# Optimization experiments

Hardware: AMD Instinct MI355X
Metric: run time of the kernel (lower is better)

The kernel has to match this reference:

```python
import jax, jax.numpy as jnp
import numpy as np

SCALES = (32.0, 64.0, 128.0, 256.0)
RATIOS = (0.5, 1.0, 2.0)
STRIDE = 16
KEEP = 2000          # pre-NMS top-k
TOPK = 300           # post-NMS top-k
MIN_SIZE = 16.0
SCORE_THRESH = 0.05
NMS_THRESH = 0.7


def static_anchors():
    a = []
    for s in SCALES:
        for r in RATIOS:
            w = s * r ** 0.5
            h = s / r ** 0.5
            a.append((-w / 2, -h / 2, w / 2, h / 2))
    return jnp.asarray(a, jnp.float32)  # [12,4]


def generate_anchors(h, w):
    base = static_anchors()
    sx = jnp.arange(w, dtype=jnp.float32) * STRIDE + STRIDE / 2
    sy = jnp.arange(h, dtype=jnp.float32) * STRIDE + STRIDE / 2
    yy, xx = jnp.meshgrid(sy, sx, indexing='ij')
    xs, ys = xx.reshape(-1), yy.reshape(-1)
    shifts = jnp.stack((xs, ys, xs, ys), axis=1)            # [HW,4]
    return (base[None, :, :] + shifts[:, None, :]).reshape(-1, 4)  # [HW*12,4]


def apply_deltas(anchors, d):
    # bbox reg weights are all 1.0
    aw = anchors[..., 2] - anchors[..., 0]
    ah = anchors[..., 3] - anchors[..., 1]
    ax = anchors[..., 0] + aw * 0.5
    ay = anchors[..., 1] + ah * 0.5
    x = ax + d[..., 0] * aw
    y = ay + d[..., 1] * ah
    w = aw * jnp.exp(d[..., 2])
    h = ah * jnp.exp(d[..., 3])
    return jnp.stack((x - w * 0.5, y - h * 0.5, x + w * 0.5, y + h * 0.5), axis=-1)


def conv2d(x, w, b, pad):
    y = jax.lax.conv_general_dilated(x, w, (1, 1), [(pad, pad), (pad, pad)],
                                     dimension_numbers=('NCHW', 'OIHW', 'NCHW'))
    return y + b[None, :, None, None]


def nms_fixed(boxes, scores, valid):
    # boxes already sorted by descending score; greedy NMS with fixed shapes.
    area = (boxes[:, 2] - boxes[:, 0]) * (boxes[:, 3] - boxes[:, 1])
    lt = jnp.maximum(boxes[:, None, :2], boxes[None, :, :2])
    rb = jnp.minimum(boxes[:, None, 2:], boxes[None, :, 2:])
    wh = jnp.clip(rb - lt, 0.0)
    inter = wh[..., 0] * wh[..., 1]
    iou = inter / jnp.maximum(area[:, None] + area[None, :] - inter, 1e-6)
    n = boxes.shape[0]

    def body(i, state):
        keep, supp = state
        k = jnp.logical_and(~supp[i], True)
        keep = keep.at[i].set(k)
        supp = jnp.logical_or(supp, jnp.logical_and(k, iou[i] > NMS_THRESH))
        return keep, supp

    keep, _ = jax.lax.fori_loop(0, n, body, (jnp.zeros(n, bool), ~valid))
    masked = jnp.where(keep, scores, -jnp.inf)
    top_s, top_i = jax.lax.top_k(masked, TOPK)
    ok = top_s > -jnp.inf
    out_boxes = jnp.where(ok[:, None], boxes[top_i], 0.0)
    out_scores = jnp.where(ok, top_s, 0.0)
    return out_boxes, out_scores


def rpn_forward(fx, w1, b1, w2, b2, w3, b3, img_h, img_w):
    _, _, H, W = fx.shape
    x = jax.nn.relu(conv2d(fx, w1, b1, 1))        # [1,512,H,W]
    ox = conv2d(x, w2, b2, 0)                     # [1,12,H,W]
    ax = conv2d(x, w3, b3, 0)                     # [1,48,H,W]
    anchors = generate_anchors(H, W)              # [A,4]
    ox = jnp.transpose(ox, (0, 2, 3, 1)).reshape(-1)                     # [A]
    ax = jnp.transpose(ax.reshape(1, 12, 4, H, W), (0, 3, 4, 1, 2)).reshape(-1, 4)  # [A,4]
    px = apply_deltas(anchors, ax)                # [A,4]
    s = jax.nn.sigmoid(ox)
    top_s, idx = jax.lax.top_k(s, KEEP)           # pre-NMS filter
    b = px[idx]
    x1 = jnp.clip(b[:, 0], 0.0, img_w)
    x2 = jnp.clip(b[:, 2], 0.0, img_w)
    y1 = jnp.clip(b[:, 1], 0.0, img_h)
    y2 = jnp.clip(b[:, 3], 0.0, img_h)
    boxes = jnp.stack((x1, y1, x2, y2), axis=1)
    valid = ((x2 - x1) >= MIN_SIZE) & ((y2 - y1) >= MIN_SIZE) & (top_s >= SCORE_THRESH)
    out_boxes, out_scores = nms_fixed(boxes, top_s, valid)
    return jnp.concatenate((out_boxes, out_scores[:, None]), axis=1)  # [TOPK,5]


def setup_inputs() -> dict:
    key = jax.random.key(0)
    ks = jax.random.split(key, 4)
    fx = jax.random.normal(ks[0], (1, 1024, 64, 64), jnp.float32)
    w1 = jax.random.normal(ks[1], (512, 1024, 3, 3), jnp.float32) * 0.01
    w2 = jax.random.normal(ks[2], (12, 512, 1, 1), jnp.float32) * 0.01
    w3 = jax.random.normal(ks[3], (48, 512, 1, 1), jnp.float32) * 0.01
    return {"fx": fx, "w1": w1, "b1": jnp.zeros((512,), jnp.float32),
            "w2": w2, "b2": jnp.zeros((12,), jnp.float32),
            "w3": w3, "b3": jnp.zeros((48,), jnp.float32),
            "img_h": 1024, "img_w": 1024}


def reference(fx, w1, b1, w2, b2, w3, b3, img_h, img_w):
    return rpn_forward(fx, w1, b1, w2, b2, w3, b3, float(img_h), float(img_w))
```

## Files before the change

kernel.cpp:

```cpp
#include <hip/hip_runtime.h>
#include <math.h>

typedef unsigned int u32;
typedef unsigned long long u64;
typedef unsigned short u16;

typedef float f32x16 __attribute__((ext_vector_type(16)));
typedef short bf16x8 __attribute__((ext_vector_type(8)));

#define A_TOTAL 49152
#define NKEEP 2000
#define NTOPK 300
#define SORTN 4096

#define OFF_PACC   0u
#define OFF_SCORES 16777216u
#define OFF_HIST   16973824u
#define OFF_KEYS   17235968u
#define OFF_CAND5  17268736u
#define OFF_MASK   17309696u
#define OFF_BOX4   17833984u
#define OFF_MISC   17899520u
#define OFF_PREW   17903616u
#define OFF_POX    17903616u
#define WS_NEED    46215168ull

__global__ __launch_bounds__(256) void k_init(u32* __restrict__ hist, u64* __restrict__ keys,
                                              u32* __restrict__ misc, float* __restrict__ out) {
    int t = blockIdx.x * 256 + threadIdx.x;
    if (t < 65536) hist[t] = 0u;
    if (t < SORTN) keys[t] = 0ull;
    if (t < NTOPK * 5) out[t] = 0.f;
    if (t == 0) misc[0] = 0u;
}

__device__ __forceinline__ u16 f2bf(float v) {
    u32 u = __float_as_uint(v);
    return (u16)((u + 0x7FFFu + ((u >> 16) & 1u)) >> 16);
}
__device__ __forceinline__ float bf2f(u16 h) { return __uint_as_float(((u32)h) << 16); }
__device__ __forceinline__ void split3(float v, u16& h, u16& m, u16& l) {
    h = f2bf(v);
    float r1 = v - bf2f(h);
    m = f2bf(r1);
    float r2 = r1 - bf2f(m);
    l = f2bf(r2);
}
__device__ __forceinline__ bf16x8 ldsfrag(const u16* p) {
    const u64* q = (const u64*)p;
    union { u64 w[2]; bf16x8 v; } x;
    x.w[0] = q[0];
    x.w[1] = q[1];
    return x.v;
}
__device__ __forceinline__ void gll16(const void* g, void* l) {
    __builtin_amdgcn_global_load_lds((const __attribute__((address_space(1))) void*)g,
                                     (__attribute__((address_space(3))) void*)l, 16, 0, 0);
}
__device__ __forceinline__ void gll4(const void* g, void* l) {
    __builtin_amdgcn_global_load_lds((const __attribute__((address_space(1))) void*)g,
                                     (__attribute__((address_space(3))) void*)l, 4, 0, 0);
}

__global__ __launch_bounds__(256) void k_splitw(const float* __restrict__ w1, uint4* __restrict__ preW) {
    __shared__ __align__(16) u16 sW[3 * 9216];
    const int tid = threadIdx.x;
    const int c = blockIdx.x;
    const int yb = blockIdx.y;
    const int kh = blockIdx.z;
    const float* base = w1 + (size_t)(yb * 64) * 9216 + (size_t)(kh * 512 + c * 16) * 9;
#pragma unroll
    for (int j = 0; j < 36; j++) {
        int e = tid + j * 256;
        int co = e / 144, r = e - co * 144;
        int ci = r / 9, tap = r - ci * 9;
        float v = base[(size_t)co * 9216 + r];
        u16 h, m, l;
        split3(v, h, m, l);
        int li = ((tap * 2 + (ci >> 3)) * 64 + co) * 8 + (ci & 7);
        sW[li] = h; sW[9216 + li] = m; sW[18432 + li] = l;
    }
    __syncthreads();
    const uint4* sw4 = (const uint4*)sW;
    uint4* dst = preW + (size_t)(((kh * 8 + yb) * 32 + c) * 3) * 1152;
#pragma unroll
    for (int j = 0; j < 14; j++) {
        int e = tid + j * 256;
        if (e < 3456) dst[e] = sw4[e];
    }
}

__global__ __launch_bounds__(512) void k_conv1m(const float* __restrict__ fx, const uint4* __restrict__ preW,
                                                float* __restrict__ pacc) {
    __shared__ __align__(16) u16 sA[3 * 9216];
    __shared__ __align__(16) u16 sB[3 * 3600];
    u32* const sB32 = (u32*)sB;
    const int tid = threadIdx.x;
    const int lane = tid & 63;
    const int wid = tid >> 6;
    const int cgw = wid >> 2;
    const int pgw = wid & 3;
    const int n = lane & 31;
    const int g = lane >> 5;
    const int bid = blockIdx.x;
    const int yb = bid & 7;
    const int rest = bid >> 3;
    const int bpx = rest & 31;
    const int kh = rest >> 5;
    const int y0 = (bpx >> 2) * 8, x0 = (bpx & 3) * 16;
    const int ci_base = kh * 512;

    int fgp[3], flp[3];
    bool wrp[3], ldp[3];
#pragma unroll
    for (int j = 0; j < 3; j++) {
        int p = tid + j * 512;
        bool wr = p < 1440;
        int a = p / 180, rem = p - a * 180;
        int hy = rem / 18, hx = rem - hy * 18;
        int gy = y0 + hy - 1, gx = x0 + hx - 1;
        bool ok = wr && gy >= 0 && gy < 64 && gx >= 0 && gx < 64;
        wrp[j] = wr;
        ldp[j] = ok;
        fgp[j] = ok ? ((2 * a) * 4096 + gy * 64 + gx) : 0;
        flp[j] = wr ? (rem * 10 + a) : 0;
    }

    f32x16 acc;
    double accD[16];
#pragma unroll
    for (int i = 0; i < 16; i++) { acc[i] = 0.f; accD[i] = 0.0; }

    float pA0[3], pA1[3], pB0[3], pB1[3];
    {
        const float* f0 = fx + (size_t)ci_base * 4096;
        const float* f1 = fx + (size_t)(ci_base + 16) * 4096;
#pragma unroll
        for (int j = 0; j < 3; j++) {
            pA0[j] = ldp[j] ? f0[fgp[j]] : 0.f;
            pA1[j] = ldp[j] ? f0[fgp[j] + 4096] : 0.f;
            pB0[j] = ldp[j] ? f1[fgp[j]] : 0.f;
            pB1[j] = ldp[j] ? f1[fgp[j] + 4096] : 0.f;
        }
    }
    const char* wbase = (const char*)preW + (size_t)((kh * 8 + yb) * 32) * 3 * 18432;
    char* const sAc = (char*)sA;

#pragma unroll 1
    for (int c = 0; c < 32; c++) {
        __syncthreads();
        const char* wsrc = wbase + (size_t)c * 3 * 18432;
#pragma unroll
        for (int s = 0; s < 3; s++) {
            gll16(wsrc + s * 18432 + tid * 16,         sAc + s * 18432 + wid * 1024);
            gll16(wsrc + s * 18432 + 8192 + tid * 16,  sAc + s * 18432 + 8192 + wid * 1024);
            gll4 (wsrc + s * 18432 + 16384 + tid * 4,  sAc + s * 18432 + 16384 + wid * 256);
        }
#pragma unroll
        for (int j = 0; j < 3; j++) {
            if (wrp[j]) {
                u16 h0, m0, l0, h1, m1, l1;
                split3(pA0[j], h0, m0, l0);
                split3(pA1[j], h1, m1, l1);
                sB32[flp[j]] = (u32)h0 | ((u32)h1 << 16);
                sB32[1800 + flp[j]] = (u32)m0 | ((u32)m1 << 16);
                sB32[3600 + flp[j]] = (u32)l0 | ((u32)l1 << 16);
            }
        }
        __syncthreads();
#pragma unroll
        for (int j = 0; j < 3; j++) { pA0[j] = pB0[j]; pA1[j] = pB1[j]; }
        if (c < 30) {
            const float* fp = fx + (size_t)(ci_base + (c + 2) * 16) * 4096;
#pragma unroll
            for (int j = 0; j < 3; j++) {
                pB0[j] = ldp[j] ? fp[fgp[j]] : 0.f;
                pB1[j] = ldp[j] ? fp[fgp[j] + 4096] : 0.f;
            }
        }

#pragma unroll 1
        for (int dy = 0; dy < 3; dy++) {
#pragma unroll
            for (int dx = 0; dx < 3; dx++) {
                const int tap = dy * 3 + dx;
                const int aoff = ((tap * 2 + g) * 64 + cgw * 32 + n) * 8;
                bf16x8 ah = ldsfrag(&sA[aoff]);
                bf16x8 am = ldsfrag(&sA[9216 + aoff]);
                bf16x8 al = ldsfrag(&sA[18432 + aoff]);
                const int loc = (pgw * 2 + (n >> 4) + dy) * 18 + (n & 15) + dx;
                const int boff = loc * 20 + g * 8;
                bf16x8 bh = ldsfrag(&sB[boff]);
                bf16x8 bm = ldsfrag(&sB[3600 + boff]);
                bf16x8 bl = ldsfrag(&sB[7200 + boff]);
                acc = __builtin_amdgcn_mfma_f32_32x32x16_bf16(ah, bh, acc, 0, 0, 0);
                acc = __builtin_amdgcn_mfma_f32_32x32x16_bf16(ah, bm, acc, 0, 0, 0);
                acc = __builtin_amdgcn_mfma_f32_32x32x16_bf16(am, bh, acc, 0, 0, 0);
                acc = __builtin_amdgcn_mfma_f32_32x32x16_bf16(ah, bl, acc, 0, 0, 0);
                acc = __builtin_amdgcn_mfma_f32_32x32x16_bf16(am, bm, acc, 0, 0, 0);
                acc = __builtin_amdgcn_mfma_f32_32x32x16_bf16(al, bh, acc, 0, 0, 0);
            }
#pragma unroll
            for (int i = 0; i < 16; i++) { accD[i] += (double)acc[i]; acc[i] = 0.f; }
        }
    }

    {
        int p = pgw * 32 + n;
        int py = p >> 4, pxx = p & 15;
        int gp = (y0 + py) * 64 + x0 + pxx;
        const int row_hi = 4 * g;
#pragma unroll
        for (int rg = 0; rg < 16; rg++) {
            int co = yb * 64 + cgw * 32 + (rg & 3) + 8 * (rg >> 2) + row_hi;
            pacc[(size_t)kh * 2097152 + (size_t)co * 4096 + gp] = (float)accD[rg];
        }
    }
}

__global__ __launch_bounds__(512) void k_conv1m_fb(const float* __restrict__ fx, const float* __restrict__ w1,
                                                   float* __restrict__ pacc) {
    __shared__ u16 sA[3 * 9472];
    __shared__ u16 sB[3 * 3600];
    u32* const sA32 = (u32*)sA;
    const int tid = threadIdx.x;
    const int lane = tid & 63;
    const int wid = tid >> 6;
    const int cgw = wid >> 2;
    const int pgw = wid & 3;
    const int n = lane & 31;
    const int g = lane >> 5;
    const int bid = blockIdx.x;
    const int yb = bid & 7;
    const int rest = bid >> 3;
    const int bpx = rest & 31;
    const int kh = rest >> 5;
    const int y0 = (bpx >> 2) * 8, x0 = (bpx & 3) * 16;
    const int co0 = yb * 64;
    const int ci_base = kh * 512;

    int wgp[9], wlp[9];
#pragma unroll
    for (int j = 0; j < 9; j++) {
        int p = tid + j * 512;
        int co = p / 72, q = p - co * 72;
        int a = q & 7, b = q >> 3;
        wgp[j] = co * 9216 + (2 * a) * 9 + b;
        wlp[j] = co * 74 + b * 8 + a;
    }
    int fg0[6], fl[6];
#pragma unroll
    for (int j = 0; j < 6; j++) {
        int idx = tid + j * 512;
        bool wr = idx < 2880;
        int ci = idx / 180, rem = idx - ci * 180;
        int hy = rem / 18, hx = rem - hy * 18;
        int gy = y0 + hy - 1, gx = x0 + hx - 1;
        bool ok = wr && gy >= 0 && gy < 64 && gx >= 0 && gx < 64;
        fg0[j] = ok ? (ci * 4096 + gy * 64 + gx) : -1;
        fl[j] = wr ? (rem * 20 + ci) : -1;
    }

    f32x16 acc;
    double accD[16];
#pragma unroll
    for (int i = 0; i < 16; i++) { acc[i] = 0.f; accD[i] = 0.0; }

    float pw[18], pfA[6], pfB[6];
    {
        const float* wp = w1 + (size_t)co0 * 9216 + (size_t)ci_base * 9;
#pragma unroll
        for (int j = 0; j < 9; j++) { pw[2 * j] = wp[wgp[j]]; pw[2 * j + 1] = wp[wgp[j] + 9]; }
        const float* f0 = fx + (size_t)ci_base * 4096;
        const float* f1 = fx + (size_t)(ci_base + 16) * 4096;
#pragma unroll
        for (int j = 0; j < 6; j++) {
            pfA[j] = (fg0[j] >= 0) ? f0[fg0[j]] : 0.f;
            pfB[j] = (fg0[j] >= 0) ? f1[fg0[j]] : 0.f;
        }
    }

#pragma unroll 1
    for (int c = 0; c < 32; c++) {
        __syncthreads();
#pragma unroll
        for (int j = 0; j < 9; j++) {
            u16 h0, m0, l0, h1, m1, l1;
            split3(pw[2 * j], h0, m0, l0);
            split3(pw[2 * j + 1], h1, m1, l1);
            sA32[wlp[j]] = (u32)h0 | ((u32)h1 << 16);
            sA32[4736 + wlp[j]] = (u32)m0 | ((u32)m1 << 16);
            sA32[9472 + wlp[j]] = (u32)l0 | ((u32)l1 << 16);
        }
#pragma unroll
        for (int j = 0; j < 6; j++) {
            if (fl[j] >= 0) {
                u16 h, m, l;
                split3(pfA[j], h, m, l);
                sB[fl[j]] = h; sB[3600 + fl[j]] = m; sB[7200 + fl[j]] = l;
            }
        }
        __syncthreads();
        if (c < 31) {
            const float* wp = w1 + (size_t)co0 * 9216 + (size_t)(ci_base + (c + 1) * 16) * 9;
#pragma unroll
            for (int j = 0; j < 9; j++) { pw[2 * j] = wp[wgp[j]]; pw[2 * j + 1] = wp[wgp[j] + 9]; }
        }
#pragma unroll
        for (int j = 0; j < 6; j++) pfA[j] = pfB[j];
        if (c < 30) {
            const float* fp = fx + (size_t)(ci_base + (c + 2) * 16) * 4096;
#pragma unroll
            for (int j = 0; j < 6; j++) pfB[j] = (fg0[j] >= 0) ? fp[fg0[j]] : 0.f;
        }

#pragma unroll 1
        for (int dy = 0; dy < 3; dy++) {
#pragma unroll
            for (int dx = 0; dx < 3; dx++) {
                const int tap = dy * 3 + dx;
                const int aoff = (cgw * 32 + n) * 148 + tap * 16 + g * 8;
                bf16x8 ah = ldsfrag(&sA[aoff]);
                bf16x8 am = ldsfrag(&sA[9472 + aoff]);
                bf16x8 al = ldsfrag(&sA[18944 + aoff]);
                const int loc = (pgw * 2 + (n >> 4) + dy) * 18 + (n & 15) + dx;
                const int boff = loc * 20 + g * 8;
                bf16x8 bh = ldsfrag(&sB[boff]);
                bf16x8 bm = ldsfrag(&sB[3600 + boff]);
                bf16x8 bl = ldsfrag(&sB[7200 + boff]);
                acc = __builtin_amdgcn_mfma_f32_32x32x16_bf16(ah, bh, acc, 0, 0, 0);
                acc = __builtin_amdgcn_mfma_f32_32x32x16_bf16(ah, bm, acc, 0, 0, 0);
                acc = __builtin_amdgcn_mfma_f32_32x32x16_bf16(am, bh, acc, 0, 0, 0);
                acc = __builtin_amdgcn_mfma_f32_32x32x16_bf16(ah, bl, acc, 0, 0, 0);
                acc = __builtin_amdgcn_mfma_f32_32x32x16_bf16(am, bm, acc, 0, 0, 0);
                acc = __builtin_amdgcn_mfma_f32_32x32x16_bf16(al, bh, acc, 0, 0, 0);
            }
#pragma unroll
            for (int i = 0; i < 16; i++) { accD[i] += (double)acc[i]; acc[i] = 0.f; }
        }
    }

    {
        int p = pgw * 32 + n;
        int py = p >> 4, pxx = p & 15;
        int gp = (y0 + py) * 64 + x0 + pxx;
        const int row_hi = 4 * g;
#pragma unroll
        for (int rg = 0; rg < 16; rg++) {
            int co = co0 + cgw * 32 + (rg & 3) + 8 * (rg >> 2) + row_hi;
            pacc[(size_t)kh * 2097152 + (size_t)co * 4096 + gp] = (float)accD[rg];
        }
    }
}

__global__ __launch_bounds__(256) void k_conv23q(const float* __restrict__ pacc,
                                                 const float* __restrict__ b1,
                                                 const float* __restrict__ w2, const float* __restrict__ w3,
                                                 double* __restrict__ pox) {
    __shared__ float xs[32 * 64];
    __shared__ float wsh[60 * 128];
    const int tid = threadIdx.x;
    const int px0 = blockIdx.x * 64;
    const int cib = blockIdx.y * 128;
    const int px = tid & 63;
    const int og = tid >> 6;

#pragma unroll
    for (int k = 0; k < 30; k++) {
        int e = tid + k * 256;
        int o = e >> 7, ci = e & 127;
        float wv = (o < 12) ? w2[o * 512 + cib + ci] : w3[(size_t)(o - 12) * 512 + cib + ci];
        wsh[o * 128 + ci] = wv;
    }

    double acc[15];
#pragma unroll
    for (int j = 0; j < 15; j++) acc[j] = 0.0;

#pragma unroll 1
    for (int ch = 0; ch < 4; ch++) {
        __syncthreads();
#pragma unroll
        for (int k = 0; k < 8; k++) {
            int e = tid + k * 256;
            int ci = e >> 6, p = e & 63;
            int cig = cib + ch * 32 + ci;
            size_t gi = (size_t)cig * 4096 + px0 + p;
            double v = (double)pacc[gi] + (double)pacc[2097152 + gi] + (double)b1[cig];
            xs[ci * 64 + p] = fmaxf((float)v, 0.f);
        }
        __syncthreads();
#pragma unroll 1
        for (int ci = 0; ci < 32; ci++) {
            double xd = (double)xs[ci * 64 + px];
            const float* wrow = &wsh[ch * 32 + ci];
#pragma unroll
            for (int j = 0; j < 15; j++)
                acc[j] = fma(xd, (double)wrow[(og * 15 + j) * 128], acc[j]);
        }
    }
#pragma unroll
    for (int j = 0; j < 15; j++) {
        int o = og * 15 + j;
        pox[((size_t)o * 4 + blockIdx.y) * 4096 + px0 + px] = acc[j];
    }
}

__global__ __launch_bounds__(256) void k_scores(const double* __restrict__ pox,
                                                const float* __restrict__ b2,
                                                float* __restrict__ scores, u32* __restrict__ hist) {
    int idx = blockIdx.x * 256 + threadIdx.x;
    if (idx >= A_TOTAL) return;
    int px = idx / 12, a = idx - px * 12;
    double t = 0.0;
#pragma unroll
    for (int q = 0; q < 4; q++) t += pox[((size_t)a * 4 + q) * 4096 + px];
    float o = (float)(t + (double)b2[a]);
    float s = (float)(1.0 / (1.0 + exp(-(double)o)));
    scores[idx] = s;
    atomicAdd(&hist[__float_as_uint(s) >> 16], 1u);
}

__global__ __launch_bounds__(256) void k_scanhist(const u32* __restrict__ hist, u32* __restrict__ misc) {
    __shared__ u32 csum[256];
    __shared__ u32 cb[256];
    __shared__ int s_cidx;
    __shared__ u32 s_cacc;
    int t = threadIdx.x;
    u32 sum = 0;
    const uint4* h4 = (const uint4*)(hist + t * 256);
    for (int j = 0; j < 64; j++) { uint4 v = h4[j]; sum += v.x + v.y + v.z + v.w; }
    csum[t] = sum;
    __syncthreads();
    if (t == 0) {
        u32 acc = 0;
        int c = 255;
        for (; c > 0; c--) {
            if (acc + csum[c] >= NKEEP) break;
            acc += csum[c];
        }
        s_cidx = c;
        s_cacc = acc;
    }
    __syncthreads();
    cb[t] = hist[s_cidx * 256 + t];
    __syncthreads();
    if (t == 0) {
        u32 acc = s_cacc;
        int b = 255;
        for (; b > 0; b--) {
            acc += cb[b];
            if (acc >= NKEEP) break;
        }
        misc[1] = (u32)(s_cidx * 256 + b);
    }
}

__global__ __launch_bounds__(256) void k_compact(const float* __restrict__ scores, u32* __restrict__ misc,
                                                 const double* __restrict__ pox, const float* __restrict__ b3,
                                                 const int* __restrict__ imh, const int* __restrict__ imw,
                                                 u64* __restrict__ keys, float* __restrict__ boxes4) {
    int idx = blockIdx.x * 256 + threadIdx.x;
    if (idx >= A_TOTAL) return;
    u32 bits = __float_as_uint(scores[idx]);
    if ((bits >> 16) < misc[1]) return;
    u32 slot = atomicAdd(&misc[0], 1u);
    if (slot >= SORTN) return;
    keys[slot] = ((u64)bits << 32) | (u64)(~(u32)idx);

    int px = idx / 12, a = idx - px * 12;
    float d[4];
#pragma unroll
    for (int c = 0; c < 4; c++) {
        int oo = 12 + a * 4 + c;
        double u = 0.0;
#pragma unroll
        for (int q = 0; q < 4; q++) u += pox[((size_t)oo * 4 + q) * 4096 + px];
        d[c] = (float)(u + (double)b3[a * 4 + c]);
    }
    int py = px >> 6, pxx = px & 63;
    double cx = pxx * 16.0 + 8.0, cy = py * 16.0 + 8.0;
    int si = a / 3, ri = a - si * 3;
    double scale = (double)(32 << si);
    double ratio = 0.5 * (double)(1 << ri);
    double sq = sqrt(ratio);
    double aw = scale * sq, ah = scale / sq;
    double xc = cx + (double)d[0] * aw;
    double yc = cy + (double)d[1] * ah;
    double wv = aw * exp((double)d[2]);
    double hv = ah * exp((double)d[3]);
    float W = (float)imw[0], H = (float)imh[0];
    boxes4[slot * 4 + 0] = fminf(fmaxf((float)(xc - wv * 0.5), 0.f), W);
    boxes4[slot * 4 + 1] = fminf(fmaxf((float)(yc - hv * 0.5), 0.f), H);
    boxes4[slot * 4 + 2] = fminf(fmaxf((float)(xc + wv * 0.5), 0.f), W);
    boxes4[slot * 4 + 3] = fminf(fmaxf((float)(yc + hv * 0.5), 0.f), H);
}

__global__ __launch_bounds__(1024) void k_sort(const u64* __restrict__ keys, const u64* __restrict__ keys_ro,
                                               const float* __restrict__ boxes4,
                                               float* __restrict__ cand5, u64* __restrict__ suppws) {
    (void)keys_ro;
    __shared__ u64 lk[SORTN];
    __shared__ u16 slotof[SORTN];
    int t = threadIdx.x;
#pragma unroll
    for (int r = 0; r < 4; r++) {
        int i = r * 1024 + t;
        lk[i] = (keys[i] & ~0xFFFFull) | (u64)(u16)i;
    }
#pragma unroll
    for (int r = 0; r < 4; r++) {
        int i = r * 1024 + t;
        lk[i] = keys[i];
        slotof[i] = (u16)i;
    }
    for (int kk = 2; kk <= SORTN; kk <<= 1) {
        for (int jj = kk >> 1; jj > 0; jj >>= 1) {
            __syncthreads();
#pragma unroll
            for (int rep = 0; rep < 4; rep++) {
                int i = rep * 1024 + t;
                int ixj = i ^ jj;
                if (ixj > i) {
                    u64 a = lk[i], b = lk[ixj];
                    bool sw = ((i & kk) == 0) ? (a < b) : (a > b);
                    if (sw) {
                        lk[i] = b; lk[ixj] = a;
                        u16 sa = slotof[i], sb = slotof[ixj];
                        slotof[i] = sb; slotof[ixj] = sa;
                    }
                }
            }
        }
    }
    __syncthreads();
#pragma unroll
    for (int rep = 0; rep < 2; rep++) {
        int i = rep * 1024 + t;
        bool suppb = true;
        float c0 = 0.f, c1 = 0.f, c2 = 0.f, c3 = 0.f, cs = 0.f;
        if (i < NKEEP) {
            u64 key = lk[i];
            cs = __uint_as_float((u32)(key >> 32));
            int slot = slotof[i];
            c0 = boxes4[slot * 4 + 0];
            c1 = boxes4[slot * 4 + 1];
            c2 = boxes4[slot * 4 + 2];
            c3 = boxes4[slot * 4 + 3];
            bool valid = ((c2 - c0) >= 16.f) && ((c3 - c1) >= 16.f) && (cs >= 0.05f);
            suppb = !valid;
        }
        cand5[i * 5 + 0] = c0;
        cand5[i * 5 + 1] = c1;
        cand5[i * 5 + 2] = c2;
        cand5[i * 5 + 3] = c3;
        cand5[i * 5 + 4] = cs;
        u64 bal = __ballot(suppb ? 1 : 0);
        if ((t & 63) == 0) suppws[i >> 6] = bal;
    }
}

__global__ __launch_bounds__(64) void k_mask(const float* __restrict__ cand5, u64* __restrict__ mask) {
    __shared__ float cb[64][5];
    int t = threadIdx.x;
    int bi = blockIdx.y, bj = blockIdx.x;
    int j = bj * 64 + t;
    {
        float b0 = cand5[j * 5 + 0], b1v = cand5[j * 5 + 1], b2v = cand5[j * 5 + 2], b3v = cand5[j * 5 + 3];
        cb[t][0] = b0; cb[t][1] = b1v; cb[t][2] = b2v; cb[t][3] = b3v;
        cb[t][4] = (b2v - b0) * (b3v - b1v);
    }
    __syncthreads();
    int i = bi * 64 + t;
    float r0 = cand5[i * 5 + 0], r1 = cand5[i * 5 + 1], r2 = cand5[i * 5 + 2], r3 = cand5[i * 5 + 3];
    float ra = (r2 - r0) * (r3 - r1);
    u64 bits = 0ull;
#pragma unroll 4
    for (int c = 0; c < 64; c++) {
        float lx = fmaxf(r0, cb[c][0]);
        float ly = fmaxf(r1, cb[c][1]);
        float rx = fminf(r2, cb[c][2]);
        float ry = fminf(r3, cb[c][3]);
        float w = fmaxf(rx - lx, 0.f);
        float h = fmaxf(ry - ly, 0.f);
        float inter = w * h;
        float iou = inter / fmaxf(ra + cb[c][4] - inter, 1e-6f);
        if (iou > 0.7f) bits |= (1ull << c);
    }
    mask[(size_t)i * 32 + bj] = bits;
}

__global__ __launch_bounds__(64) void k_scan(const u64* __restrict__ mask, const float* __restrict__ cand5,
                                             const u64* __restrict__ suppws, float* __restrict__ out) {
    int lane = threadIdx.x;
    u64 supp = (lane < 32) ? suppws[lane] : 0ull;
    u64 bufA[8], bufB[8];
    float dA[8], dB[8];
#pragma unroll
    for (int k = 0; k < 8; k++) {
        bufA[k] = (lane < 32) ? mask[(size_t)k * 32 + lane] : 0ull;
        dA[k] = (lane < 5) ? cand5[k * 5 + lane] : 0.f;
    }
    int kcount = 0;
    for (int gq = 0; gq < 256; gq++) {
        int base = gq * 8;
        if (gq < 255) {
            int nb = base + 8;
#pragma unroll
            for (int k = 0; k < 8; k++) {
                bufB[k] = (lane < 32) ? mask[(size_t)(nb + k) * 32 + lane] : 0ull;
                dB[k] = (lane < 5) ? cand5[(nb + k) * 5 + lane] : 0.f;
            }
        }
        int w = gq >> 3;
        u64 cur = __shfl(supp, w);
#pragma unroll
        for (int k = 0; k < 8; k++) {
            int i = base + k;
            if (i < NKEEP && !((cur >> (i & 63)) & 1ull)) {
                if (kcount < NTOPK) {
                    if (lane < 5) out[kcount * 5 + lane] = dA[k];
                    kcount++;
                }
                supp |= bufA[k];
                cur |= __shfl(bufA[k], w);
            }
        }
        if (kcount >= NTOPK) return;
#pragma unroll
        for (int k = 0; k < 8; k++) { bufA[k] = bufB[k]; dA[k] = dB[k]; }
    }
}

extern "C" void kernel_launch(void* const* d_in, const int* in_sizes, int n_in,
                              void* d_out, int out_size, void* d_ws, size_t ws_size,
                              hipStream_t stream) {
    (void)in_sizes; (void)n_in; (void)out_size;
    const float* fx = (const float*)d_in[0];
    const float* w1 = (const float*)d_in[1];
    const float* b1 = (const float*)d_in[2];
    const float* w2 = (const float*)d_in[3];
    const float* b2 = (const float*)d_in[4];
    const float* w3 = (const float*)d_in[5];
    const float* b3 = (const float*)d_in[6];
    const int* imh = (const int*)d_in[7];
    const int* imw = (const int*)d_in[8];

    char* ws = (char*)d_ws;
    float*  pacc   = (float*)(ws + OFF_PACC);
    float*  scores = (float*)(ws + OFF_SCORES);
    u32*    hist   = (u32*)(ws + OFF_HIST);
    u64*    keys   = (u64*)(ws + OFF_KEYS);
    float*  cand5  = (float*)(ws + OFF_CAND5);
    u64*    mask   = (u64*)(ws + OFF_MASK);
    float*  boxes4 = (float*)(ws + OFF_BOX4);
    u32*    misc   = (u32*)(ws + OFF_MISC);
    u64*    suppws = (u64*)(ws + OFF_MISC + 64);
    uint4*  preW   = (uint4*)(ws + OFF_PREW);
    double* pox    = (double*)(ws + OFF_POX);
    float*  out    = (float*)d_out;

    k_init<<<256, 256, 0, stream>>>(hist, keys, misc, out);
    if (ws_size >= WS_NEED) {
        k_splitw<<<dim3(32, 8, 2), 256, 0, stream>>>(w1, preW);
        k_conv1m<<<512, 512, 0, stream>>>(fx, preW, pacc);
    } else {
        k_conv1m_fb<<<512, 512, 0, stream>>>(fx, w1, pacc);
    }
    k_conv23q<<<dim3(64, 4), 256, 0, stream>>>(pacc, b1, w2, w3, pox);
    k_scores<<<192, 256, 0, stream>>>(pox, b2, scores, hist);
    k_scanhist<<<1, 256, 0, stream>>>(hist, misc);
    k_compact<<<192, 256, 0, stream>>>(scores, misc, pox, b3, imh, imw, keys, boxes4);
    k_sort<<<1, 1024, 0, stream>>>(keys, keys, boxes4, cand5, suppws);
    k_mask<<<dim3(32, 32), 64, 0, stream>>>(cand5, mask);
    k_scan<<<1, 64, 0, stream>>>(mask, cand5, suppws, out);
}
```

Before: 478.3 us.

## Give each conv wave two output-channel tiles and size the bitonic sort to the candidate count

The main conv kernel now uses 256 threads per block. Each wave computes both 32-row output-channel halves, so every loaded B fragment feeds two accumulators and B LDS reads are halved. Per-thread staging work and registers double (two double accumulator sets), which may lower occupancy. The sort kernel also reads the candidate count and sorts only 2048 elements when that is enough, and a redundant key-initialisation loop is removed.

```diff
diff --git a/kernel.cpp b/kernel.cpp
--- a/kernel.cpp
+++ b/kernel.cpp
@@ -90,16 +90,14 @@
     }
 }
 
-__global__ __launch_bounds__(512) void k_conv1m(const float* __restrict__ fx, const uint4* __restrict__ preW,
+__global__ __launch_bounds__(256) void k_conv1m(const float* __restrict__ fx, const uint4* __restrict__ preW,
                                                 float* __restrict__ pacc) {
     __shared__ __align__(16) u16 sA[3 * 9216];
     __shared__ __align__(16) u16 sB[3 * 3600];
     u32* const sB32 = (u32*)sB;
     const int tid = threadIdx.x;
     const int lane = tid & 63;
-    const int wid = tid >> 6;
-    const int cgw = wid >> 2;
-    const int pgw = wid & 3;
+    const int pgw = tid >> 6;
     const int n = lane & 31;
     const int g = lane >> 5;
     const int bid = blockIdx.x;
@@ -110,11 +108,11 @@
     const int y0 = (bpx >> 2) * 8, x0 = (bpx & 3) * 16;
     const int ci_base = kh * 512;
 
-    int fgp[3], flp[3];
-    bool wrp[3], ldp[3];
-#pragma unroll
-    for (int j = 0; j < 3; j++) {
-        int p = tid + j * 512;
+    int fgp[6], flp[6];
+    bool wrp[6], ldp[6];
+#pragma unroll
+    for (int j = 0; j < 6; j++) {
+        int p = tid + j * 256;
         bool wr = p < 1440;
         int a = p / 180, rem = p - a * 180;
         int hy = rem / 18, hx = rem - hy * 18;
@@ -126,17 +124,17 @@
         flp[j] = wr ? (rem * 10 + a) : 0;
     }
 
-    f32x16 acc;
-    double accD[16];
-#pragma unroll
-    for (int i = 0; i < 16; i++) { acc[i] = 0.f; accD[i] = 0.0; }
-
-    float pA0[3], pA1[3], pB0[3], pB1[3];
+    f32x16 acc0, acc1;
+    double accD0[16], accD1[16];
+#pragma unroll
+    for (int i = 0; i < 16; i++) { acc0[i] = 0.f; acc1[i] = 0.f; accD0[i] = 0.0; accD1[i] = 0.0; }
+
+    float pA0[6], pA1[6], pB0[6], pB1[6];
     {
         const float* f0 = fx + (size_t)ci_base * 4096;
         const float* f1 = fx + (size_t)(ci_base + 16) * 4096;
 #pragma unroll
-        for (int j = 0; j < 3; j++) {
+        for (int j = 0; j < 6; j++) {
             pA0[j] = ldp[j] ? f0[fgp[j]] : 0.f;
             pA1[j] = ldp[j] ? f0[fgp[j] + 4096] : 0.f;
             pB0[j] = ldp[j] ? f1[fgp[j]] : 0.f;
@@ -152,12 +150,17 @@
         const char* wsrc = wbase + (size_t)c * 3 * 18432;
 #pragma unroll
         for (int s = 0; s < 3; s++) {
-            gll16(wsrc + s * 18432 + tid * 16,         sAc + s * 18432 + wid * 1024);
-            gll16(wsrc + s * 18432 + 8192 + tid * 16,  sAc + s * 18432 + 8192 + wid * 1024);
-            gll4 (wsrc + s * 18432 + 16384 + tid * 4,  sAc + s * 18432 + 16384 + wid * 256);
-        }
-#pragma unroll
-        for (int j = 0; j < 3; j++) {
+            const char* ws_ = wsrc + s * 18432;
+            char* ls_ = sAc + s * 18432;
+            gll16(ws_ + tid * 16,          ls_ + pgw * 1024);
+            gll16(ws_ + 4096 + tid * 16,   ls_ + 4096 + pgw * 1024);
+            gll16(ws_ + 8192 + tid * 16,   ls_ + 8192 + pgw * 1024);
+            gll16(ws_ + 12288 + tid * 16,  ls_ + 12288 + pgw * 1024);
+            gll4 (ws_ + 16384 + tid * 4,   ls_ + 16384 + pgw * 256);
+            gll4 (ws_ + 17408 + tid * 4,   ls_ + 17408 + pgw * 256);
+        }
+#pragma unroll
+        for (int j = 0; j < 6; j++) {
             if (wrp[j]) {
                 u16 h0, m0, l0, h1, m1, l1;
                 split3(pA0[j], h0, m0, l0);
@@ -169,11 +172,11 @@
         }
         __syncthreads();
 #pragma unroll
-        for (int j = 0; j < 3; j++) { pA0[j] = pB0[j]; pA1[j] = pB1[j]; }
+        for (int j = 0; j < 6; j++) { pA0[j] = pB0[j]; pA1[j] = pB1[j]; }
         if (c < 30) {
             const float* fp = fx + (size_t)(ci_base + (c + 2) * 16) * 4096;
 #pragma unroll
-            for (int j = 0; j < 3; j++) {
+            for (int j = 0; j < 6; j++) {
                 pB0[j] = ldp[j] ? fp[fgp[j]] : 0.f;
                 pB1[j] = ldp[j] ? fp[fgp[j] + 4096] : 0.f;
             }
@@ -184,24 +187,36 @@
 #pragma unroll
             for (int dx = 0; dx < 3; dx++) {
                 const int tap = dy * 3 + dx;
-                const int aoff = ((tap * 2 + g) * 64 + cgw * 32 + n) * 8;
-                bf16x8 ah = ldsfrag(&sA[aoff]);
-                bf16x8 am = ldsfrag(&sA[9216 + aoff]);
-                bf16x8 al = ldsfrag(&sA[18432 + aoff]);
+                const int aoff = ((tap * 2 + g) * 64 + n) * 8;
+                bf16x8 ah0 = ldsfrag(&sA[aoff]);
+                bf16x8 am0 = ldsfrag(&sA[9216 + aoff]);
+                bf16x8 al0 = ldsfrag(&sA[18432 + aoff]);
+                bf16x8 ah1 = ldsfrag(&sA[aoff + 256]);
+                bf16x8 am1 = ldsfrag(&sA[9216 + aoff + 256]);
+                bf16x8 al1 = ldsfrag(&sA[18432 + aoff + 256]);
                 const int loc = (pgw * 2 + (n >> 4) + dy) * 18 + (n & 15) + dx;
                 const int boff = loc * 20 + g * 8;
                 bf16x8 bh = ldsfrag(&sB[boff]);
                 bf16x8 bm = ldsfrag(&sB[3600 + boff]);
                 bf16x8 bl = ldsfrag(&sB[7200 + boff]);
-                acc = __builtin_amdgcn_mfma_f32_32x32x16_bf16(ah, bh, acc, 0, 0, 0);
-                acc = __builtin_amdgcn_mfma_f32_32x32x16_bf16(ah, bm, acc, 0, 0, 0);
-                acc = __builtin_amdgcn_mfma_f32_32x32x16_bf16(am, bh, acc, 0, 0, 0);
-                acc = __builtin_amdgcn_mfma_f32_32x32x16_bf16(ah, bl, acc, 0, 0, 0);
-                acc = __builtin_amdgcn_mfma_f32_32x32x16_bf16(am, bm, acc, 0, 0, 0);
-                acc = __builtin_amdgcn_mfma_f32_32x32x16_bf16(al, bh, acc, 0, 0, 0);
-            }
-#pragma unroll
-            for (int i = 0; i < 16; i++) { accD[i] += (double)acc[i]; acc[i] = 0.f; }
+                acc0 = __builtin_amdgcn_mfma_f32_32x32x16_bf16(ah0, bh, acc0, 0, 0, 0);
+                acc1 = __builtin_amdgcn_mfma_f32_32x32x16_bf16(ah1, bh, acc1, 0, 0, 0);
+                acc0 = __builtin_amdgcn_mfma_f32_32x32x16_bf16(ah0, bm, acc0, 0, 0, 0);
+                acc1 = __builtin_amdgcn_mfma_f32_32x32x16_bf16(ah1, bm, acc1, 0, 0, 0);
+                acc0 = __builtin_amdgcn_mfma_f32_32x32x16_bf16(am0, bh, acc0, 0, 0, 0);
+                acc1 = __builtin_amdgcn_mfma_f32_32x32x16_bf16(am1, bh, acc1, 0, 0, 0);
+                acc0 = __builtin_amdgcn_mfma_f32_32x32x16_bf16(ah0, bl, acc0, 0, 0, 0);
+                acc1 = __builtin_amdgcn_mfma_f32_32x32x16_bf16(ah1, bl, acc1, 0, 0, 0);
+                acc0 = __builtin_amdgcn_mfma_f32_32x32x16_bf16(am0, bm, acc0, 0, 0, 0);
+                acc1 = __builtin_amdgcn_mfma_f32_32x32x16_bf16(am1, bm, acc1, 0, 0, 0);
+                acc0 = __builtin_amdgcn_mfma_f32_32x32x16_bf16(al0, bh, acc0, 0, 0, 0);
+                acc1 = __builtin_amdgcn_mfma_f32_32x32x16_bf16(al1, bh, acc1, 0, 0, 0);
+            }
+#pragma unroll
+            for (int i = 0; i < 16; i++) {
+                accD0[i] += (double)acc0[i]; acc0[i] = 0.f;
+                accD1[i] += (double)acc1[i]; acc1[i] = 0.f;
+            }
         }
     }
 
@@ -212,8 +227,9 @@
         const int row_hi = 4 * g;
 #pragma unroll
         for (int rg = 0; rg < 16; rg++) {
-            int co = yb * 64 + cgw * 32 + (rg & 3) + 8 * (rg >> 2) + row_hi;
-            pacc[(size_t)kh * 2097152 + (size_t)co * 4096 + gp] = (float)accD[rg];
+            int cob = yb * 64 + (rg & 3) + 8 * (rg >> 2) + row_hi;
+            pacc[(size_t)kh * 2097152 + (size_t)cob * 4096 + gp] = (float)accD0[rg];
+            pacc[(size_t)kh * 2097152 + (size_t)(cob + 32) * 4096 + gp] = (float)accD1[rg];
         }
     }
 }
@@ -496,29 +512,24 @@
     boxes4[slot * 4 + 3] = fminf(fmaxf((float)(yc + hv * 0.5), 0.f), H);
 }
 
-__global__ __launch_bounds__(1024) void k_sort(const u64* __restrict__ keys, const u64* __restrict__ keys_ro,
+__global__ __launch_bounds__(1024) void k_sort(const u64* __restrict__ keys, const u32* __restrict__ misc,
                                                const float* __restrict__ boxes4,
                                                float* __restrict__ cand5, u64* __restrict__ suppws) {
-    (void)keys_ro;
     __shared__ u64 lk[SORTN];
     __shared__ u16 slotof[SORTN];
     int t = threadIdx.x;
-#pragma unroll
-    for (int r = 0; r < 4; r++) {
-        int i = r * 1024 + t;
-        lk[i] = (keys[i] & ~0xFFFFull) | (u64)(u16)i;
-    }
-#pragma unroll
-    for (int r = 0; r < 4; r++) {
+    u32 count = misc[0];
+    const int N = (count <= 2048u) ? 2048 : SORTN;
+    const int reps = N >> 10;
+    for (int r = 0; r < reps; r++) {
         int i = r * 1024 + t;
         lk[i] = keys[i];
         slotof[i] = (u16)i;
     }
-    for (int kk = 2; kk <= SORTN; kk <<= 1) {
+    for (int kk = 2; kk <= N; kk <<= 1) {
         for (int jj = kk >> 1; jj > 0; jj >>= 1) {
             __syncthreads();
-#pragma unroll
-            for (int rep = 0; rep < 4; rep++) {
+            for (int rep = 0; rep < reps; rep++) {
                 int i = rep * 1024 + t;
                 int ixj = i ^ jj;
                 if (ixj > i) {
@@ -663,7 +674,7 @@
     k_init<<<256, 256, 0, stream>>>(hist, keys, misc, out);
     if (ws_size >= WS_NEED) {
         k_splitw<<<dim3(32, 8, 2), 256, 0, stream>>>(w1, preW);
-        k_conv1m<<<512, 512, 0, stream>>>(fx, preW, pacc);
+        k_conv1m<<<512, 256, 0, stream>>>(fx, preW, pacc);
     } else {
         k_conv1m_fb<<<512, 512, 0, stream>>>(fx, w1, pacc);
     }
@@ -671,7 +682,7 @@
     k_scores<<<192, 256, 0, stream>>>(pox, b2, scores, hist);
     k_scanhist<<<1, 256, 0, stream>>>(hist, misc);
     k_compact<<<192, 256, 0, stream>>>(scores, misc, pox, b3, imh, imw, keys, boxes4);
-    k_sort<<<1, 1024, 0, stream>>>(keys, keys, boxes4, cand5, suppws);
+    k_sort<<<1, 1024, 0, stream>>>(keys, misc, boxes4, cand5, suppws);
     k_mask<<<dim3(32, 32), 64, 0, stream>>>(cand5, mask);
     k_scan<<<1, 64, 0, stream>>>(mask, cand5, suppws, out);
 }
```

Result: slower. 490.9 us (+2.6%).
